# Performance work log

Measured on AMD Instinct MI355X. Metric: run time of the kernel, lower is better.

Reference implementation:

```python
import jax, jax.numpy as jnp
import numpy as np

B, T, D = 4, 4096, 1024

def setup_inputs() -> dict:
    key = jax.random.key(0)
    ks = jax.random.split(key, 8)
    s = 1.0 / np.sqrt(D)
    return {
        "x": jax.random.normal(ks[0], (B, T, D), dtype=jnp.float32),
        # diagonal SSM params (per-channel)
        "A": jax.random.uniform(ks[1], (D,), dtype=jnp.float32, minval=0.5, maxval=0.99),  # stable decay
        "Bp": jax.random.normal(ks[2], (D,), dtype=jnp.float32) * 0.1,
        "Cp": jax.random.normal(ks[3], (D,), dtype=jnp.float32),
        # gate Linear
        "gate_w": jax.random.uniform(ks[4], (D, D), dtype=jnp.float32, minval=-s, maxval=s),
        "gate_b": jnp.zeros((D,), dtype=jnp.float32),
        # out Linear
        "out_w": jax.random.uniform(ks[5], (D, D), dtype=jnp.float32, minval=-s, maxval=s),
        "out_b": jnp.zeros((D,), dtype=jnp.float32),
    }

def _ssm(x, A, Bp, Cp):
    # diagonal linear recurrence: h_t = A*h_{t-1} + Bp*x_t ; y_t = Cp*h_t
    bx = x * Bp  # (B,T,D)
    def step(h, bx_t):
        h = A * h + bx_t  # (B,D)
        return h, h
    h0 = jnp.zeros((x.shape[0], x.shape[2]), dtype=x.dtype)
    _, hs = jax.lax.scan(step, h0, jnp.swapaxes(bx, 0, 1))  # (T,B,D)
    return jnp.swapaxes(hs, 0, 1) * Cp  # (B,T,D)

def reference(x, A, Bp, Cp, gate_w, gate_b, out_w, out_b):
    ssm_out = _ssm(x, A, Bp, Cp)
    gate = jax.nn.sigmoid(jnp.einsum('btd,ed->bte', x, gate_w) + gate_b)
    y = gate * ssm_out
    return jnp.einsum('btd,ed->bte', y, out_w) + out_b
```

## Files before the change

kernel.cpp:

```cpp
#include <hip/hip_runtime.h>
#include <hip/hip_bf16.h>
#include <cstdio>

typedef __hip_bfloat16 bf16;
typedef __bf16 bf16x8 __attribute__((ext_vector_type(8)));
typedef float f32x4 __attribute__((ext_vector_type(4)));

#define B_DIM 4
#define T_DIM 4096
#define D_DIM 1024
#define NC 64
#define LC 64

#define M_DIM (B_DIM * T_DIM)
#define BM 256
#define BN 256
#define BK 32
#define NT (D_DIM / BK)
#define GM (M_DIM / BM)
#define GN (D_DIM / BN)

__global__ __launch_bounds__(256) void cast_w_kernel(
    const float* __restrict__ gw, const float* __restrict__ ow,
    bf16* __restrict__ gw16, bf16* __restrict__ ow16, int n) {
  int i = blockIdx.x * 256 + threadIdx.x;
  if (i < n) {
    gw16[i] = __float2bfloat16(gw[i]);
    ow16[i] = __float2bfloat16(ow[i]);
  }
}

__global__ __launch_bounds__(256) void ssm_pass1(
    const float* __restrict__ x, const float* __restrict__ A,
    const float* __restrict__ Bp, float* __restrict__ hfin) {
  const int tid  = threadIdx.x;
  const int dblk = blockIdx.x & 3;
  const int c    = (blockIdx.x >> 2) & (NC - 1);
  const int b    = blockIdx.x >> 8;
  const int d    = dblk * 256 + tid;
  const float a = A[d], bp = Bp[d];
  const float* p = x + ((size_t)(b * T_DIM + c * LC) * D_DIM + d);
  float h = 0.f;
#pragma unroll 4
  for (int i = 0; i < LC; ++i)
    h = fmaf(a, h, bp * p[(size_t)i * D_DIM]);
  hfin[(b * NC + c) * D_DIM + d] = h;
}

__global__ __launch_bounds__(256) void ssm_pass2(
    const float* __restrict__ A, const float* __restrict__ hfin,
    float* __restrict__ hin) {
  const int idx = blockIdx.x * 256 + threadIdx.x;
  const int d = idx & (D_DIM - 1);
  const int b = idx >> 10;
  float aL = A[d];
#pragma unroll
  for (int s = 0; s < 6; ++s) aL *= aL;
  float h = 0.f;
  for (int c = 0; c < NC; ++c) {
    const int o = (b * NC + c) * D_DIM + d;
    hin[o] = h;
    h = fmaf(aL, h, hfin[o]);
  }
}

__global__ __launch_bounds__(256) void ssm_pass3(
    const float* __restrict__ x, const float* __restrict__ A,
    const float* __restrict__ Bp, const float* __restrict__ Cp,
    const float* __restrict__ hin, bf16* __restrict__ ssm16,
    bf16* __restrict__ x16) {
  const int tid  = threadIdx.x;
  const int dblk = blockIdx.x & 3;
  const int c    = (blockIdx.x >> 2) & (NC - 1);
  const int b    = blockIdx.x >> 8;
  const int d    = dblk * 256 + tid;
  const float a = A[d], bp = Bp[d], cp = Cp[d];
  float h = hin[(b * NC + c) * D_DIM + d];
  const size_t base = (size_t)(b * T_DIM + c * LC) * D_DIM + d;
#pragma unroll 4
  for (int i = 0; i < LC; ++i) {
    const size_t o = base + (size_t)i * D_DIM;
    const float xv = x[o];
    h = fmaf(a, h, bp * xv);
    ssm16[o] = __float2bfloat16(cp * h);
    x16[o]  = __float2bfloat16(xv);
  }
}

template <bool GATE>
__global__ __launch_bounds__(512) void gemm256(
    const bf16* __restrict__ Xm, const bf16* __restrict__ Wm,
    const float* __restrict__ bias, const bf16* __restrict__ ssm,
    bf16* __restrict__ Ybf, float* __restrict__ Yf) {
  __shared__ __align__(16) short LDS[4][16384];

  const int tid  = threadIdx.x;
  const int lane = tid & 63;
  const int wave = tid >> 6;
  const int wm = wave >> 2;
  const int wn = wave & 3;
  const int l15 = lane & 15;
  const int sA = ((lane >> 4) ^ ((l15 >> 1) & 3)) << 3;

  const int bid = blockIdx.x;
  const int swz = (bid & 7) * (GM * GN / 8) + (bid >> 3);
  const int m0 = (swz >> 2) * BM;
  const int n0 = (swz & 3) * BN;

  const int row0 = tid >> 2;
  const int c0   = (tid & 3) ^ ((row0 >> 1) & 3);
  const size_t offA0 = (size_t)(m0 + row0) * D_DIM + c0 * 8;
  const size_t offB0 = (size_t)(n0 + row0) * D_DIM + c0 * 8;

  auto gll = [](const bf16* g, short* l) {
    __builtin_amdgcn_global_load_lds(
        (const __attribute__((address_space(1))) void*)g,
        (__attribute__((address_space(3))) void*)l, 16, 0, 0);
  };
  auto STAGE = [&](int buf, int kt) {
    const size_t ko = (size_t)kt * BK;
    short* b0 = &LDS[buf][0] + wave * 512;
    gll(Xm + offA0 + ko,               b0);
    gll(Xm + offA0 + 128 * D_DIM + ko, b0 + 4096);
    gll(Wm + offB0 + ko,               b0 + 8192);
    gll(Wm + offB0 + 128 * D_DIM + ko, b0 + 12288);
  };

  f32x4 acc[8][4] = {};

  STAGE(0, 0);
  STAGE(1, 1);
  STAGE(2, 2);
  asm volatile("s_waitcnt vmcnt(8)" ::: "memory");
  __builtin_amdgcn_s_barrier();

#define KTILE_BODY(T_, VMSTR, DO_STAGE, DO_BAR)                             \
  {                                                                         \
    const short* bb = &LDS[(T_) & 3][0];                                    \
    bf16x8 a[8], b[4];                                                      \
    _Pragma("unroll")                                                       \
    for (int i = 0; i < 8; ++i)                                             \
      a[i] = *(const bf16x8*)(bb + (wm * 128 + i * 16 + l15) * BK + sA);    \
    _Pragma("unroll")                                                       \
    for (int j = 0; j < 4; ++j)                                             \
      b[j] = *(const bf16x8*)(bb + 8192 + (wn * 64 + j * 16 + l15) * BK + sA); \
    if (DO_STAGE) STAGE(((T_) + 3) & 3, (T_) + 3);                          \
    asm volatile("s_waitcnt lgkmcnt(0)" ::: "memory");                      \
    __builtin_amdgcn_sched_barrier(0);                                      \
    __builtin_amdgcn_s_setprio(1);                                          \
    _Pragma("unroll")                                                       \
    for (int i = 0; i < 4; ++i)                                             \
      _Pragma("unroll")                                                     \
      for (int j = 0; j < 4; ++j)                                           \
        acc[i][j] =                                                         \
            __builtin_amdgcn_mfma_f32_16x16x32_bf16(a[i], b[j], acc[i][j], 0, 0, 0); \
    __builtin_amdgcn_s_setprio(0);                                          \
    if (DO_BAR) {                                                           \
      asm volatile("s_waitcnt " VMSTR ::: "memory");                        \
      __builtin_amdgcn_s_barrier();                                         \
    }                                                                       \
    __builtin_amdgcn_s_setprio(1);                                          \
    _Pragma("unroll")                                                       \
    for (int i = 4; i < 8; ++i)                                             \
      _Pragma("unroll")                                                     \
      for (int j = 0; j < 4; ++j)                                           \
        acc[i][j] =                                                         \
            __builtin_amdgcn_mfma_f32_16x16x32_bf16(a[i], b[j], acc[i][j], 0, 0, 0); \
    __builtin_amdgcn_s_setprio(0);                                          \
  }

  for (int t = 0; t < NT - 3; ++t)
    KTILE_BODY(t, "vmcnt(8)", true, true);
  KTILE_BODY(NT - 3, "vmcnt(4)", false, true);
  KTILE_BODY(NT - 2, "vmcnt(0)", false, true);
  KTILE_BODY(NT - 1, "vmcnt(0)", false, false);
#undef KTILE_BODY

#pragma unroll
  for (int i = 0; i < 8; ++i) {
#pragma unroll
    for (int j = 0; j < 4; ++j) {
      const int col = n0 + wn * 64 + j * 16 + l15;
      const float bv = bias[col];
#pragma unroll
      for (int v = 0; v < 4; ++v) {
        const int row = m0 + wm * 128 + i * 16 + (lane >> 4) * 4 + v;
        const size_t o = (size_t)row * D_DIM + col;
        const float val = acc[i][j][v] + bv;
        if (GATE) {
          const float g = 1.f / (1.f + expf(-val));
          Ybf[o] = __float2bfloat16(g * __bfloat162float(ssm[o]));
        } else {
          Yf[o] = val;
        }
      }
    }
  }
}

extern "C" void kernel_launch(void* const* d_in, const int* in_sizes, int n_in,
                              void* d_out, int out_size, void* d_ws, size_t ws_size,
                              hipStream_t stream) {
  const float* x  = (const float*)d_in[0];
  const float* A  = (const float*)d_in[1];
  const float* Bp = (const float*)d_in[2];
  const float* Cp = (const float*)d_in[3];
  const float* gw = (const float*)d_in[4];
  const float* gb = (const float*)d_in[5];
  const float* ow = (const float*)d_in[6];
  const float* ob = (const float*)d_in[7];
  float* out = (float*)d_out;

  const size_t NEED = 73400320;
  if (ws_size < NEED) {
    fprintf(stderr, "kernel_launch: ws_size %zu < needed %zu\n", ws_size, NEED);
    return;
  }
  char* ws = (char*)d_ws;
  bf16*  x16   = (bf16*)(ws);
  bf16*  ssm16 = (bf16*)(ws + 33554432);
  bf16*  gw16  = (bf16*)(ws + 67108864);
  bf16*  ow16  = (bf16*)(ws + 69206016);
  float* hfin  = (float*)(ws + 71303168);
  float* hin   = (float*)(ws + 72351744);

  cast_w_kernel<<<(D_DIM * D_DIM) / 256, 256, 0, stream>>>(gw, ow, gw16, ow16, D_DIM * D_DIM);
  ssm_pass1<<<B_DIM * NC * (D_DIM / 256), 256, 0, stream>>>(x, A, Bp, hfin);
  ssm_pass2<<<(B_DIM * D_DIM) / 256, 256, 0, stream>>>(A, hfin, hin);
  ssm_pass3<<<B_DIM * NC * (D_DIM / 256), 256, 0, stream>>>(x, A, Bp, Cp, hin, ssm16, x16);

  gemm256<true><<<GM * GN, 512, 0, stream>>>(x16, gw16, gb, ssm16, ssm16, nullptr);
  gemm256<false><<<GM * GN, 512, 0, stream>>>(ssm16, ow16, ob, nullptr, nullptr, out);
}
```

Baseline: 130.3 us.

## Shrink GEMM tile to 128x256 with 4 waves and triple-buffered LDS

Reduces the GEMM block tile from 256x256 with 8 waves to 128x256 with 4 waves. Each wave now covers all 128 rows and a 64-column slice. The LDS pipeline drops from 4 stages to 3 (72 KB per block instead of 128 KB), and launch bounds request 2 blocks per CU so two blocks can share a CU and hide latency. The cost is twice as many blocks, and each B tile is reloaded by twice as many blocks, which raises global and L2 traffic. The prefetch depth is also shorter.

New measurement: 137.0 us. 5.2% more time.

```diff
diff --git a/kernel.cpp b/kernel.cpp
--- a/kernel.cpp
+++ b/kernel.cpp
@@ -13,7 +13,7 @@
 #define LC 64
 
 #define M_DIM (B_DIM * T_DIM)
-#define BM 256
+#define BM 128
 #define BN 256
 #define BK 32
 #define NT (D_DIM / BK)
@@ -88,17 +88,15 @@
 }
 
 template <bool GATE>
-__global__ __launch_bounds__(512) void gemm256(
+__global__ __launch_bounds__(256, 2) void gemm128(
     const bf16* __restrict__ Xm, const bf16* __restrict__ Wm,
     const float* __restrict__ bias, const bf16* __restrict__ ssm,
     bf16* __restrict__ Ybf, float* __restrict__ Yf) {
-  __shared__ __align__(16) short LDS[4][16384];
+  __shared__ __align__(16) short LDS[3][12288];
 
   const int tid  = threadIdx.x;
   const int lane = tid & 63;
   const int wave = tid >> 6;
-  const int wm = wave >> 2;
-  const int wn = wave & 3;
   const int l15 = lane & 15;
   const int sA = ((lane >> 4) ^ ((l15 >> 1) & 3)) << 3;
 
@@ -109,8 +107,13 @@
 
   const int row0 = tid >> 2;
   const int c0   = (tid & 3) ^ ((row0 >> 1) & 3);
-  const size_t offA0 = (size_t)(m0 + row0) * D_DIM + c0 * 8;
-  const size_t offB0 = (size_t)(n0 + row0) * D_DIM + c0 * 8;
+  size_t offA[2], offB[4];
+#pragma unroll
+  for (int it = 0; it < 2; ++it)
+    offA[it] = (size_t)(m0 + it * 64 + row0) * D_DIM + c0 * 8;
+#pragma unroll
+  for (int it = 0; it < 4; ++it)
+    offB[it] = (size_t)(n0 + it * 64 + row0) * D_DIM + c0 * 8;
 
   auto gll = [](const bf16* g, short* l) {
     __builtin_amdgcn_global_load_lds(
@@ -119,32 +122,32 @@
   };
   auto STAGE = [&](int buf, int kt) {
     const size_t ko = (size_t)kt * BK;
-    short* b0 = &LDS[buf][0] + wave * 512;
-    gll(Xm + offA0 + ko,               b0);
-    gll(Xm + offA0 + 128 * D_DIM + ko, b0 + 4096);
-    gll(Wm + offB0 + ko,               b0 + 8192);
-    gll(Wm + offB0 + 128 * D_DIM + ko, b0 + 12288);
+#pragma unroll
+    for (int it = 0; it < 2; ++it)
+      gll(Xm + offA[it] + ko, &LDS[buf][(it * 256 + wave * 64) * 8]);
+#pragma unroll
+    for (int it = 0; it < 4; ++it)
+      gll(Wm + offB[it] + ko, &LDS[buf][4096 + (it * 256 + wave * 64) * 8]);
   };
 
   f32x4 acc[8][4] = {};
 
   STAGE(0, 0);
   STAGE(1, 1);
-  STAGE(2, 2);
-  asm volatile("s_waitcnt vmcnt(8)" ::: "memory");
+  asm volatile("s_waitcnt vmcnt(6)" ::: "memory");
   __builtin_amdgcn_s_barrier();
 
-#define KTILE_BODY(T_, VMSTR, DO_STAGE, DO_BAR)                             \
+#define KTILE_BODY(RB_, SB_, KT2_, VMSTR, DO_STAGE, DO_BAR)                 \
   {                                                                         \
-    const short* bb = &LDS[(T_) & 3][0];                                    \
+    const short* bb = &LDS[RB_][0];                                         \
     bf16x8 a[8], b[4];                                                      \
     _Pragma("unroll")                                                       \
     for (int i = 0; i < 8; ++i)                                             \
-      a[i] = *(const bf16x8*)(bb + (wm * 128 + i * 16 + l15) * BK + sA);    \
+      a[i] = *(const bf16x8*)(bb + (i * 16 + l15) * BK + sA);               \
     _Pragma("unroll")                                                       \
     for (int j = 0; j < 4; ++j)                                             \
-      b[j] = *(const bf16x8*)(bb + 8192 + (wn * 64 + j * 16 + l15) * BK + sA); \
-    if (DO_STAGE) STAGE(((T_) + 3) & 3, (T_) + 3);                          \
+      b[j] = *(const bf16x8*)(bb + 4096 + (wave * 64 + j * 16 + l15) * BK + sA); \
+    if (DO_STAGE) STAGE(SB_, KT2_);                                         \
     asm volatile("s_waitcnt lgkmcnt(0)" ::: "memory");                      \
     __builtin_amdgcn_sched_barrier(0);                                      \
     __builtin_amdgcn_s_setprio(1);                                          \
@@ -169,22 +172,27 @@
     __builtin_amdgcn_s_setprio(0);                                          \
   }
 
-  for (int t = 0; t < NT - 3; ++t)
-    KTILE_BODY(t, "vmcnt(8)", true, true);
-  KTILE_BODY(NT - 3, "vmcnt(4)", false, true);
-  KTILE_BODY(NT - 2, "vmcnt(0)", false, true);
-  KTILE_BODY(NT - 1, "vmcnt(0)", false, false);
+  {
+    int rb = 0;
+    for (int t = 0; t < NT - 2; ++t) {
+      int sb = rb + 2; if (sb >= 3) sb -= 3;
+      KTILE_BODY(rb, sb, t + 2, "vmcnt(6)", true, true);
+      ++rb; if (rb == 3) rb = 0;
+    }
+  }
+  KTILE_BODY((NT - 2) % 3, 0, 0, "vmcnt(0)", false, true);
+  KTILE_BODY((NT - 1) % 3, 0, 0, "vmcnt(0)", false, false);
 #undef KTILE_BODY
 
 #pragma unroll
   for (int i = 0; i < 8; ++i) {
 #pragma unroll
     for (int j = 0; j < 4; ++j) {
-      const int col = n0 + wn * 64 + j * 16 + l15;
+      const int col = n0 + wave * 64 + j * 16 + l15;
       const float bv = bias[col];
 #pragma unroll
       for (int v = 0; v < 4; ++v) {
-        const int row = m0 + wm * 128 + i * 16 + (lane >> 4) * 4 + v;
+        const int row = m0 + i * 16 + (lane >> 4) * 4 + v;
         const size_t o = (size_t)row * D_DIM + col;
         const float val = acc[i][j][v] + bv;
         if (GATE) {
@@ -229,6 +237,6 @@
   ssm_pass2<<<(B_DIM * D_DIM) / 256, 256, 0, stream>>>(A, hfin, hin);
   ssm_pass3<<<B_DIM * NC * (D_DIM / 256), 256, 0, stream>>>(x, A, Bp, Cp, hin, ssm16, x16);
 
-  gemm256<true><<<GM * GN, 512, 0, stream>>>(x16, gw16, gb, ssm16, ssm16, nullptr);
-  gemm256<false><<<GM * GN, 512, 0, stream>>>(ssm16, ow16, ob, nullptr, nullptr, out);
-}
+  gemm128<true><<<GM * GN, 256, 0, stream>>>(x16, gw16, gb, ssm16, ssm16, nullptr);
+  gemm128<false><<<GM * GN, 256, 0, stream>>>(ssm16, ow16, ob, nullptr, nullptr, out);
+}
```
